# Kernel tuning notes

Measured on AMD Instinct MI355X. Metric: run time of the kernel, lower is better.

## Reference

```python
import jax, jax.numpy as jnp
import numpy as np

CODE_DIMS = [256, 512, 1024, 2048]
C = 256
BETA = 0.25
B = 64
N = 1024


def setup_inputs() -> dict:
    key = jax.random.key(0)
    ks = jax.random.split(key, 2 + len(CODE_DIMS))
    z_e = jax.random.normal(ks[0], (B, N, C), dtype=jnp.float32)
    expert_idx = jax.random.randint(ks[1], (B,), 0, len(CODE_DIMS))
    s = 1.0 / np.sqrt(C)  # torch uniform init bound
    inp = {"z_e": z_e, "expert_idx": expert_idx}
    for r, K in enumerate(CODE_DIMS):
        inp[f"cb{r}"] = jax.random.uniform(ks[2 + r], (K, C), minval=-s, maxval=s, dtype=jnp.float32)
    return inp


def _vq_expert(z_e, cb):
    # z_e: [B, N, C], cb: [K, C]
    Bz, Nz, Cz = z_e.shape
    zf = z_e.reshape(-1, Cz)                                  # [B*N, C]
    dists = ((zf ** 2).sum(axis=1, keepdims=True)
             + (cb ** 2).sum(axis=1)[None, :]
             - 2.0 * zf @ cb.T)                               # [B*N, K]
    idx = jnp.argmin(dists, axis=1)                           # [B*N]
    z_q = cb[idx].reshape(Bz, Nz, Cz)                         # [B, N, C]
    return z_q, idx.reshape(Bz, Nz)


def reference(z_e, expert_idx, cb0, cb1, cb2, cb3):
    cbs = [cb0, cb1, cb2, cb3]
    Bz, Nz, Cz = z_e.shape
    sg = jax.lax.stop_gradient
    z_q_out = jnp.zeros_like(z_e)
    indices = jnp.zeros((Bz, Nz), dtype=jnp.int32)
    vq_loss = jnp.asarray(0.0, dtype=z_e.dtype)
    for r, cb in enumerate(cbs):
        z_q, idx = _vq_expert(z_e, cb)
        mask = expert_idx == r                                # [B]
        mf = mask.astype(z_e.dtype)[:, None, None]            # [B,1,1]
        cnt = mask.sum().astype(z_e.dtype)
        denom = jnp.maximum(cnt * Nz * Cz, 1.0)               # mean over masked subset
        codebook_loss = jnp.sum(mf * (sg(z_q) - z_e) ** 2) / denom
        commit_loss = jnp.sum(mf * (z_q - sg(z_e)) ** 2) / denom
        loss_r = (codebook_loss + BETA * commit_loss) / Cz
        frac = cnt / Bz                                       # z_in.numel()/z_e.numel()
        vq_loss = vq_loss + frac * loss_r
        z_q_st = z_e + sg(z_q - z_e)                          # straight-through
        z_q_out = jnp.where(mf > 0, z_q_st, z_q_out)
        indices = jnp.where(mask[:, None], idx.astype(jnp.int32), indices)
    return z_q_out, indices, vq_loss
```

## Files before the change

### kernel.cpp

```cpp
#include <hip/hip_runtime.h>
#include <hip/hip_bf16.h>


#define EPS_GAP 2e-3f
#define NTOK 65536

typedef __attribute__((ext_vector_type(8))) short bf16x8;
typedef __attribute__((ext_vector_type(4))) float f32x4;

__device__ inline unsigned short f2bf(float f) {
  __hip_bfloat16 h = __float2bfloat16(f);
  unsigned short u;
  __builtin_memcpy(&u, &h, 2);
  return u;
}
__device__ inline float bf2f(unsigned short u) {
  return __uint_as_float(((unsigned)u) << 16);
}

__device__ inline void gll16(const unsigned short* g, unsigned short* l) {
  __builtin_amdgcn_global_load_lds(
      (const __attribute__((address_space(1))) unsigned int*)g,
      (__attribute__((address_space(3))) unsigned int*)l, 16, 0, 0);
}

__global__ __launch_bounds__(256) void csum_split_kernel(
    const float* __restrict__ cb0, const float* __restrict__ cb1,
    const float* __restrict__ cb2, const float* __restrict__ cb3,
    float* __restrict__ csums, double* __restrict__ csums64,
    unsigned short* __restrict__ cb_hi, unsigned short* __restrict__ cb_lo,
    int* __restrict__ wl_cnt) {
  if (blockIdx.x == 0 && threadIdx.x == 0) wl_cnt[0] = 0;
  int row = blockIdx.x * 4 + (threadIdx.x >> 6);
  int lane = threadIdx.x & 63;
  const float* src; int r;
  if (row < 256)       { src = cb0; r = row; }
  else if (row < 768)  { src = cb1; r = row - 256; }
  else if (row < 1792) { src = cb2; r = row - 768; }
  else                 { src = cb3; r = row - 1792; }
  float4 v = ((const float4*)(src + r * 256))[lane];
  unsigned short h0 = f2bf(v.x), h1 = f2bf(v.y), h2 = f2bf(v.z), h3 = f2bf(v.w);
  unsigned short l0 = f2bf(v.x - bf2f(h0)), l1 = f2bf(v.y - bf2f(h1));
  unsigned short l2 = f2bf(v.z - bf2f(h2)), l3 = f2bf(v.w - bf2f(h3));
  *(ushort4*)(cb_hi + (size_t)row * 256 + lane * 4) = make_ushort4(h0, h1, h2, h3);
  *(ushort4*)(cb_lo + (size_t)row * 256 + lane * 4) = make_ushort4(l0, l1, l2, l3);
  double s = (double)v.x*v.x + (double)v.y*v.y + (double)v.z*v.z + (double)v.w*v.w;
  #pragma unroll
  for (int off = 32; off >= 1; off >>= 1) s += __shfl_down(s, off, 64);
  if (lane == 0) { csums[row] = (float)s; csums64[row] = s; }
}

__global__ __launch_bounds__(256) void ze_split_kernel(
    const float* __restrict__ z, unsigned short* __restrict__ ze_hi,
    unsigned short* __restrict__ ze_lo, double* __restrict__ parts) {
  const float4* p = (const float4*)z;
  uint2* hi = (uint2*)ze_hi;
  uint2* lo = (uint2*)ze_lo;
  const int n4 = 4194304;
  double s = 0.0;
  for (int i = blockIdx.x * 256 + threadIdx.x; i < n4; i += 256 * 1024) {
    float4 v = p[i];
    unsigned hxy, hzw, lxy, lzw;
    asm("v_cvt_pk_bf16_f32 %0, %1, %2" : "=v"(hxy) : "v"(v.x), "v"(v.y));
    asm("v_cvt_pk_bf16_f32 %0, %1, %2" : "=v"(hzw) : "v"(v.z), "v"(v.w));
    float lx = v.x - __uint_as_float(hxy << 16);
    float ly = v.y - __uint_as_float(hxy & 0xffff0000u);
    float lz = v.z - __uint_as_float(hzw << 16);
    float lw = v.w - __uint_as_float(hzw & 0xffff0000u);
    asm("v_cvt_pk_bf16_f32 %0, %1, %2" : "=v"(lxy) : "v"(lx), "v"(ly));
    asm("v_cvt_pk_bf16_f32 %0, %1, %2" : "=v"(lzw) : "v"(lz), "v"(lw));
    hi[i] = make_uint2(hxy, hzw);
    lo[i] = make_uint2(lxy, lzw);
    s += (double)v.x*(double)v.x + (double)v.y*(double)v.y
       + (double)v.z*(double)v.z + (double)v.w*(double)v.w;
  }
  #pragma unroll
  for (int off = 32; off >= 1; off >>= 1) s += __shfl_down(s, off, 64);
  __shared__ double sh[4];
  if ((threadIdx.x & 63) == 0) sh[threadIdx.x >> 6] = s;
  __syncthreads();
  if (threadIdx.x == 0) parts[blockIdx.x] = sh[0] + sh[1] + sh[2] + sh[3];
}

__global__ __launch_bounds__(512, 4) void vq_mfma(
    const unsigned short* __restrict__ ze_hi, const unsigned short* __restrict__ ze_lo,
    const int* __restrict__ expert_idx,
    const unsigned short* __restrict__ cb_hi, const unsigned short* __restrict__ cb_lo,
    const float* __restrict__ csums,
    float* __restrict__ D1, int* __restrict__ K1, float* __restrict__ D2) {
  const int b  = blockIdx.y;
  const int e  = expert_idx[b];
  const int hc = blockIdx.z;
  if (hc >= (2 << e)) return;
  const int cs_off = (e == 0) ? 0 : (e == 1) ? 256 : (e == 2) ? 768 : 1792;
  const int krow0  = cs_off + hc * 128;
  const int t0     = b * 1024 + blockIdx.x * 128;

  __shared__ unsigned short smem[2 * 2 * 128 * 32];
  __shared__ float sh_cs[128];

  const int tid = threadIdx.x;
  if (tid < 128) sh_cs[tid] = csums[krow0 + tid];

  const int w = tid >> 6, l = tid & 63;
  const int h = w >> 1, q = w & 1;
  const int m16 = l & 15, g = l >> 4;

  const int srow   = w * 16 + (l >> 2);
  const int schunk = (l & 3) ^ ((srow >> 1) & 3);
  const size_t bsrc = (size_t)(krow0 + srow) * 256 + (size_t)schunk * 8;
  const int wslot = w * 512;

  const size_t a0 = (size_t)(t0 + h * 32 + m16) * 256 + (size_t)g * 8;
  const size_t a1 = a0 + 16 * 256;

  f32x4 acc[2][4];
  #pragma unroll
  for (int i = 0; i < 2; ++i)
    #pragma unroll
    for (int j = 0; j < 4; ++j) acc[i][j] = (f32x4){0.f, 0.f, 0.f, 0.f};

  bf16x8 pAh0, pAl0, pAh1, pAl1;
  bf16x8 qAh0, qAl0, qAh1, qAl1;

  pAh0 = *(const bf16x8*)(ze_hi + a0);
  pAl0 = *(const bf16x8*)(ze_lo + a0);
  pAh1 = *(const bf16x8*)(ze_hi + a1);
  pAl1 = *(const bf16x8*)(ze_lo + a1);
  gll16(cb_hi + bsrc, smem + wslot);
  gll16(cb_lo + bsrc, smem + 4096 + wslot);

#define VQ_STEP(KP, AH0, AL0, AH1, AL1, NH0, NL0, NH1, NL1)             \
  {                                                                     \
    unsigned short* buf_ = smem + ((KP) & 1) * 8192;                    \
    if ((KP) < 7) {                                                     \
      const int kcn_ = ((KP) + 1) * 32;                                 \
      unsigned short* nb_ = smem + (((KP) + 1) & 1) * 8192;             \
      gll16(cb_hi + bsrc + kcn_, nb_ + wslot);                          \
      gll16(cb_lo + bsrc + kcn_, nb_ + 4096 + wslot);                   \
      NH0 = *(const bf16x8*)(ze_hi + a0 + kcn_);                        \
      NL0 = *(const bf16x8*)(ze_lo + a0 + kcn_);                        \
      NH1 = *(const bf16x8*)(ze_hi + a1 + kcn_);                        \
      NL1 = *(const bf16x8*)(ze_lo + a1 + kcn_);                        \
      __builtin_amdgcn_sched_barrier(0);                                \
      asm volatile("s_waitcnt vmcnt(6)" ::: "memory");                  \
    } else {                                                            \
      asm volatile("s_waitcnt vmcnt(0)" ::: "memory");                  \
    }                                                                   \
    __builtin_amdgcn_s_barrier();                                       \
    _Pragma("unroll")                                                   \
    for (int j = 0; j < 4; ++j) {                                       \
      int row_ = q * 64 + j * 16 + m16;                                 \
      int n_ = row_ * 32 + ((g ^ ((row_ >> 1) & 3)) << 3);              \
      bf16x8 bh_ = *(bf16x8*)(buf_ + n_);                               \
      bf16x8 bl_ = *(bf16x8*)(buf_ + 4096 + n_);                        \
      acc[0][j] = __builtin_amdgcn_mfma_f32_16x16x32_bf16(bh_, AH0, acc[0][j], 0, 0, 0); \
      acc[0][j] = __builtin_amdgcn_mfma_f32_16x16x32_bf16(bl_, AH0, acc[0][j], 0, 0, 0); \
      acc[0][j] = __builtin_amdgcn_mfma_f32_16x16x32_bf16(bh_, AL0, acc[0][j], 0, 0, 0); \
      acc[1][j] = __builtin_amdgcn_mfma_f32_16x16x32_bf16(bh_, AH1, acc[1][j], 0, 0, 0); \
      acc[1][j] = __builtin_amdgcn_mfma_f32_16x16x32_bf16(bl_, AH1, acc[1][j], 0, 0, 0); \
      acc[1][j] = __builtin_amdgcn_mfma_f32_16x16x32_bf16(bh_, AL1, acc[1][j], 0, 0, 0); \
    }                                                                   \
    __builtin_amdgcn_sched_barrier(0);                                  \
    __builtin_amdgcn_s_barrier();                                       \
  }

  VQ_STEP(0, pAh0, pAl0, pAh1, pAl1, qAh0, qAl0, qAh1, qAl1)
  VQ_STEP(1, qAh0, qAl0, qAh1, qAl1, pAh0, pAl0, pAh1, pAl1)
  VQ_STEP(2, pAh0, pAl0, pAh1, pAl1, qAh0, qAl0, qAh1, qAl1)
  VQ_STEP(3, qAh0, qAl0, qAh1, qAl1, pAh0, pAl0, pAh1, pAl1)
  VQ_STEP(4, pAh0, pAl0, pAh1, pAl1, qAh0, qAl0, qAh1, qAl1)
  VQ_STEP(5, qAh0, qAl0, qAh1, qAl1, pAh0, pAl0, pAh1, pAl1)
  VQ_STEP(6, pAh0, pAl0, pAh1, pAl1, qAh0, qAl0, qAh1, qAl1)
  VQ_STEP(7, qAh0, qAl0, qAh1, qAl1, pAh0, pAl0, pAh1, pAl1)
#undef VQ_STEP

  __syncthreads();
  float* mD = (float*)smem;
  int*   mK = (int*)(smem + 512);
  float* mS = (float*)(smem + 1024);

  float cst[16];
  #pragma unroll
  for (int j = 0; j < 4; ++j)
    #pragma unroll
    for (int r = 0; r < 4; ++r)
      cst[j * 4 + r] = sh_cs[q * 64 + j * 16 + g * 4 + r];

  #pragma unroll
  for (int i = 0; i < 2; ++i) {
    float bv = 3.4e38f, sv = 3.4e38f; int bk = 0;
    #pragma unroll
    for (int j = 0; j < 4; ++j) {
      #pragma unroll
      for (int r = 0; r < 4; ++r) {
        float d = fmaf(-2.0f, acc[i][j][r], cst[j * 4 + r]);
        int   c = q * 64 + j * 16 + g * 4 + r;
        if (d < bv) { sv = bv; bv = d; bk = c; }
        else        { sv = fminf(sv, d); }
      }
    }
    #pragma unroll
    for (int off = 16; off <= 32; off <<= 1) {
      float ov = __shfl_xor(bv, off);
      int   ok = __shfl_xor(bk, off);
      float os = __shfl_xor(sv, off);
      float nb; int nk;
      if (ov < bv || (ov == bv && ok < bk)) { nb = ov; nk = ok; }
      else                                  { nb = bv; nk = bk; }
      sv = fminf(fmaxf(bv, ov), fminf(sv, os));
      bv = nb; bk = nk;
    }
    if (g == 0) {
      int tloc = h * 32 + i * 16 + m16;
      mD[tloc * 2 + q] = bv;
      mK[tloc * 2 + q] = bk;
      mS[tloc * 2 + q] = sv;
    }
  }
  __syncthreads();
  if (tid < 128) {
    float B = 3.4e38f, S = 3.4e38f; int Kb = 0;
    #pragma unroll
    for (int c = 0; c < 2; ++c) {
      float d1v = mD[tid * 2 + c];
      int   k1v = mK[tid * 2 + c];
      float d2v = mS[tid * 2 + c];
      S = fminf(fmaxf(B, d1v), fminf(S, d2v));
      if (d1v < B) { B = d1v; Kb = k1v; }
    }
    int tg = t0 + tid;
    D1[hc * NTOK + tg] = B;
    K1[hc * NTOK + tg] = hc * 128 + Kb;
    D2[hc * NTOK + tg] = S;
  }
}

__global__ __launch_bounds__(256) void combine_kernel(
    const int* __restrict__ expert_idx,
    const float* __restrict__ D1, const int* __restrict__ K1,
    const float* __restrict__ D2,
    const float* __restrict__ cb0, const float* __restrict__ cb1,
    const float* __restrict__ cb2, const float* __restrict__ cb3,
    float* __restrict__ idx_out,
    int* __restrict__ wl, int* __restrict__ wl_cnt,
    double* __restrict__ parts, float* __restrict__ zq_out) {
  __shared__ int sh_idx[256];
  __shared__ double shp[4];
  const int bid = blockIdx.x;
  const int t = bid * 256 + threadIdx.x;
  const int e = expert_idx[bid >> 2];
  const int nch = 2 << e;
  float B = 3.4e38f, S = 3.4e38f; int Kb = 0;
  for (int c = 0; c < nch; ++c) {
    float d1 = D1[c * NTOK + t];
    int   k1 = K1[c * NTOK + t];
    float d2 = D2[c * NTOK + t];
    S = fminf(fmaxf(B, d1), fminf(S, d2));
    if (d1 < B) { B = d1; Kb = k1; }
  }
  idx_out[t] = (float)Kb;
  sh_idx[threadIdx.x] = Kb;
  if (S - B < EPS_GAP) {
    int p = atomicAdd(wl_cnt, 1);
    wl[p] = t;
  }
  double s = (double)B;
  #pragma unroll
  for (int off = 32; off >= 1; off >>= 1) s += __shfl_down(s, off, 64);
  if ((threadIdx.x & 63) == 0) shp[threadIdx.x >> 6] = s;
  __syncthreads();
  if (threadIdx.x == 0) parts[bid] = shp[0] + shp[1] + shp[2] + shp[3];

  const float* cb = (e == 0) ? cb0 : (e == 1) ? cb1 : (e == 2) ? cb2 : cb3;
  const int wid = threadIdx.x >> 6, lane = threadIdx.x & 63;
  for (int it = 0; it < 64; ++it) {
    int tl = it * 4 + wid;
    int row = sh_idx[tl];
    ((float4*)(zq_out + (size_t)(bid * 256 + tl) * 256))[lane] =
        ((const float4*)(cb + (size_t)row * 256))[lane];
  }
}

__global__ __launch_bounds__(256) void rescue_kernel(
    const float* __restrict__ z_e, const int* __restrict__ expert_idx,
    const float* __restrict__ cb0, const float* __restrict__ cb1,
    const float* __restrict__ cb2, const float* __restrict__ cb3,
    const double* __restrict__ csums64,
    const int* __restrict__ wl, const int* __restrict__ wl_cnt,
    float* __restrict__ zq_out, float* __restrict__ idx_out) {
  __shared__ float  szrow[256];
  __shared__ double szs[4];
  __shared__ float  sdv[3][256];
  __shared__ int    skv[3][256];
  __shared__ int    s_kc;
  const int tid = threadIdx.x;
  const int wid = tid >> 6, lane = tid & 63;
  const int n = wl_cnt[0];
  for (int it = blockIdx.x; it < n; it += gridDim.x) {
    const int t = wl[it];
    const int b = t >> 10;
    const int e = expert_idx[b];
    const int K = 256 << e;
    const float* cb = (e == 0) ? cb0 : (e == 1) ? cb1 : (e == 2) ? cb2 : cb3;
    const int off = (e == 0) ? 0 : (e == 1) ? 256 : (e == 2) ? 768 : 1792;
    const double* cs64 = csums64 + off;

    __syncthreads();
    float zv = z_e[(size_t)t * 256 + tid];
    szrow[tid] = zv;
    double zsq = (double)zv * (double)zv;
    #pragma unroll
    for (int o = 32; o >= 1; o >>= 1) zsq += __shfl_down(zsq, o, 64);
    if (lane == 0) szs[wid] = zsq;
    __syncthreads();
    const float zs_mid = (float)(szs[0] + szs[1] + szs[2] + szs[3]);
    const unsigned zu = __float_as_uint(zs_mid);
    float zs[3] = {__uint_as_float(zu - 1), zs_mid, __uint_as_float(zu + 1)};

    float bd[3] = {3.4e38f, 3.4e38f, 3.4e38f};
    int   bk[3] = {1 << 30, 1 << 30, 1 << 30};
    const float4* z4 = (const float4*)szrow;
    for (int k = tid; k < K; k += 256) {
      const float4* c4 = (const float4*)(cb + (size_t)k * 256);
      double d0 = 0.0, d1v = 0.0, d2v = 0.0, d3 = 0.0;
      for (int qq = 0; qq < 64; qq += 4) {
        float4 a0 = z4[qq],     c0 = c4[qq];
        float4 a1 = z4[qq + 1], c1 = c4[qq + 1];
        float4 a2 = z4[qq + 2], c2 = c4[qq + 2];
        float4 a3 = z4[qq + 3], c3 = c4[qq + 3];
        d0 += (double)a0.x*c0.x + (double)a0.y*c0.y + (double)a0.z*c0.z + (double)a0.w*c0.w;
        d1v+= (double)a1.x*c1.x + (double)a1.y*c1.y + (double)a1.z*c1.z + (double)a1.w*c1.w;
        d2v+= (double)a2.x*c2.x + (double)a2.y*c2.y + (double)a2.z*c2.z + (double)a2.w*c2.w;
        d3 += (double)a3.x*c3.x + (double)a3.y*c3.y + (double)a3.z*c3.z + (double)a3.w*c3.w;
      }
      double dot = (d0 + d1v) + (d2v + d3);
      const float c32 = (float)cs64[k];
      const float m2d = (float)(2.0 * dot);
      #pragma unroll
      for (int v = 0; v < 3; ++v) {
        float T1  = zs[v] + c32;
        float d32 = T1 - m2d;
        if (d32 < bd[v]) { bd[v] = d32; bk[v] = k; }
      }
    }
    #pragma unroll
    for (int v = 0; v < 3; ++v) { sdv[v][tid] = bd[v]; skv[v][tid] = bk[v]; }
    __syncthreads();
    for (int s = 128; s >= 1; s >>= 1) {
      if (tid < s) {
        #pragma unroll
        for (int v = 0; v < 3; ++v) {
          float od = sdv[v][tid + s]; int ok = skv[v][tid + s];
          if (od < sdv[v][tid] || (od == sdv[v][tid] && ok < skv[v][tid])) {
            sdv[v][tid] = od; skv[v][tid] = ok;
          }
        }
      }
      __syncthreads();
    }
    if (tid == 0) {
      int k0 = skv[0][0], k1 = skv[1][0], k2 = skv[2][0];
      int kc = (k0 == k2) ? k0 : k1;
      s_kc = kc;
      idx_out[t] = (float)kc;
    }
    __syncthreads();
    const int kc = s_kc;
    if (tid < 64)
      ((float4*)(zq_out + (size_t)t * 256))[tid] =
          ((const float4*)(cb + (size_t)kc * 256))[tid];
  }
}

__global__ __launch_bounds__(256) void finalize_kernel(
    const double* __restrict__ parts_comb, const double* __restrict__ parts_zsq,
    float* __restrict__ loss_out) {
  const int tid = threadIdx.x;
  double s = parts_comb[tid] + parts_zsq[tid] + parts_zsq[tid + 256]
           + parts_zsq[tid + 512] + parts_zsq[tid + 768];
  #pragma unroll
  for (int off = 32; off >= 1; off >>= 1) s += __shfl_down(s, off, 64);
  __shared__ double sh[4];
  if ((tid & 63) == 0) sh[tid >> 6] = s;
  __syncthreads();
  if (tid == 0)
    loss_out[0] = (float)((sh[0] + sh[1] + sh[2] + sh[3]) * (1.25 / 4294967296.0));
}

extern "C" void kernel_launch(void* const* d_in, const int* in_sizes, int n_in,
                              void* d_out, int out_size, void* d_ws, size_t ws_size,
                              hipStream_t stream) {
  const float* z_e  = (const float*)d_in[0];
  const int*   eidx = (const int*)d_in[1];
  const float* cb0  = (const float*)d_in[2];
  const float* cb1  = (const float*)d_in[3];
  const float* cb2  = (const float*)d_in[4];
  const float* cb3  = (const float*)d_in[5];

  float* zq    = (float*)d_out;
  float* idxf  = (float*)d_out + 16777216;
  float* lossf = (float*)d_out + 16777216 + 65536;

  unsigned short* ze_hi = (unsigned short*)d_out;
  unsigned short* ze_lo = ze_hi + 16777216;

  char* wsp = (char*)d_ws;
  double*         parts_comb = (double*)wsp;           wsp += 256 * 8;
  double*         parts_zsq  = (double*)wsp;           wsp += 1024 * 8;
  double*         csums64    = (double*)wsp;           wsp += 3840 * 8;
  float*          csums      = (float*)wsp;            wsp += 3840 * 4;
  int*            wl_cnt     = (int*)wsp;              wsp += 16;
  int*            wl         = (int*)wsp;              wsp += NTOK * 4;
  unsigned short* cb_hi      = (unsigned short*)wsp;   wsp += 3840 * 256 * 2;
  unsigned short* cb_lo      = (unsigned short*)wsp;   wsp += 3840 * 256 * 2;
  float*          D1         = (float*)wsp;            wsp += 16 * NTOK * 4;
  int*            K1         = (int*)wsp;              wsp += 16 * NTOK * 4;
  float*          D2         = (float*)wsp;            wsp += 16 * NTOK * 4;

  csum_split_kernel<<<960, 256, 0, stream>>>(cb0, cb1, cb2, cb3,
                                             csums, csums64, cb_hi, cb_lo, wl_cnt);
  ze_split_kernel<<<1024, 256, 0, stream>>>(z_e, ze_hi, ze_lo, parts_zsq);
  dim3 grid(8, 64, 16);
  vq_mfma<<<grid, 512, 0, stream>>>(ze_hi, ze_lo, eidx, cb_hi, cb_lo, csums, D1, K1, D2);
  combine_kernel<<<256, 256, 0, stream>>>(eidx, D1, K1, D2, cb0, cb1, cb2, cb3,
                                          idxf, wl, wl_cnt, parts_comb, zq);
  rescue_kernel<<<2048, 256, 0, stream>>>(z_e, eidx, cb0, cb1, cb2, cb3,
                                          csums64, wl, wl_cnt, zq, idxf);
  finalize_kernel<<<1, 256, 0, stream>>>(parts_comb, parts_zsq, lossf);
}
```

Before: 403.1 us.

## Bucket rescue worklist per expert and batch eight tokens per block

The near-tie worklist is now split into per-expert buckets, so the rescue kernel handles eight tokens that share a codebook in each block. Every codebook row it loads from global memory is reused across those eight tokens instead of being fetched once per token. In exchange it adds a serial per-block z-squared sum, eight sequential block reductions per batch, and larger register arrays that may lower occupancy. The grid is also halved.

```diff
diff --git a/kernel.cpp b/kernel.cpp
--- a/kernel.cpp
+++ b/kernel.cpp
@@ -30,7 +30,7 @@
     float* __restrict__ csums, double* __restrict__ csums64,
     unsigned short* __restrict__ cb_hi, unsigned short* __restrict__ cb_lo,
     int* __restrict__ wl_cnt) {
-  if (blockIdx.x == 0 && threadIdx.x == 0) wl_cnt[0] = 0;
+  if (blockIdx.x == 0 && threadIdx.x < 4) wl_cnt[threadIdx.x] = 0;
   int row = blockIdx.x * 4 + (threadIdx.x >> 6);
   int lane = threadIdx.x & 63;
   const float* src; int r;
@@ -262,8 +262,8 @@
   idx_out[t] = (float)Kb;
   sh_idx[threadIdx.x] = Kb;
   if (S - B < EPS_GAP) {
-    int p = atomicAdd(wl_cnt, 1);
-    wl[p] = t;
+    int p = atomicAdd(wl_cnt + e, 1);
+    wl[e * NTOK + p] = t;
   }
   double s = (double)B;
   #pragma unroll
@@ -283,93 +283,120 @@
 }
 
 __global__ __launch_bounds__(256) void rescue_kernel(
-    const float* __restrict__ z_e, const int* __restrict__ expert_idx,
+    const float* __restrict__ z_e,
     const float* __restrict__ cb0, const float* __restrict__ cb1,
     const float* __restrict__ cb2, const float* __restrict__ cb3,
     const double* __restrict__ csums64,
     const int* __restrict__ wl, const int* __restrict__ wl_cnt,
     float* __restrict__ zq_out, float* __restrict__ idx_out) {
-  __shared__ float  szrow[256];
-  __shared__ double szs[4];
+  __shared__ float  szrow[8 * 256];
+  __shared__ double szs[8];
+  __shared__ int    stok[8];
   __shared__ float  sdv[3][256];
   __shared__ int    skv[3][256];
   __shared__ int    s_kc;
   const int tid = threadIdx.x;
-  const int wid = tid >> 6, lane = tid & 63;
-  const int n = wl_cnt[0];
-  for (int it = blockIdx.x; it < n; it += gridDim.x) {
-    const int t = wl[it];
-    const int b = t >> 10;
-    const int e = expert_idx[b];
+
+  for (int e = 0; e < 4; ++e) {
+    const int n_e = wl_cnt[e];
+    if (n_e == 0) continue;
     const int K = 256 << e;
     const float* cb = (e == 0) ? cb0 : (e == 1) ? cb1 : (e == 2) ? cb2 : cb3;
     const int off = (e == 0) ? 0 : (e == 1) ? 256 : (e == 2) ? 768 : 1792;
     const double* cs64 = csums64 + off;
-
-    __syncthreads();
-    float zv = z_e[(size_t)t * 256 + tid];
-    szrow[tid] = zv;
-    double zsq = (double)zv * (double)zv;
-    #pragma unroll
-    for (int o = 32; o >= 1; o >>= 1) zsq += __shfl_down(zsq, o, 64);
-    if (lane == 0) szs[wid] = zsq;
-    __syncthreads();
-    const float zs_mid = (float)(szs[0] + szs[1] + szs[2] + szs[3]);
-    const unsigned zu = __float_as_uint(zs_mid);
-    float zs[3] = {__uint_as_float(zu - 1), zs_mid, __uint_as_float(zu + 1)};
-
-    float bd[3] = {3.4e38f, 3.4e38f, 3.4e38f};
-    int   bk[3] = {1 << 30, 1 << 30, 1 << 30};
-    const float4* z4 = (const float4*)szrow;
-    for (int k = tid; k < K; k += 256) {
-      const float4* c4 = (const float4*)(cb + (size_t)k * 256);
-      double d0 = 0.0, d1v = 0.0, d2v = 0.0, d3 = 0.0;
-      for (int qq = 0; qq < 64; qq += 4) {
-        float4 a0 = z4[qq],     c0 = c4[qq];
-        float4 a1 = z4[qq + 1], c1 = c4[qq + 1];
-        float4 a2 = z4[qq + 2], c2 = c4[qq + 2];
-        float4 a3 = z4[qq + 3], c3 = c4[qq + 3];
-        d0 += (double)a0.x*c0.x + (double)a0.y*c0.y + (double)a0.z*c0.z + (double)a0.w*c0.w;
-        d1v+= (double)a1.x*c1.x + (double)a1.y*c1.y + (double)a1.z*c1.z + (double)a1.w*c1.w;
-        d2v+= (double)a2.x*c2.x + (double)a2.y*c2.y + (double)a2.z*c2.z + (double)a2.w*c2.w;
-        d3 += (double)a3.x*c3.x + (double)a3.y*c3.y + (double)a3.z*c3.z + (double)a3.w*c3.w;
+    const int nb = (n_e + 7) >> 3;
+
+    for (int bi = blockIdx.x; bi < nb; bi += gridDim.x) {
+      const int m = min(8, n_e - bi * 8);
+      __syncthreads();
+      if (tid < 8) stok[tid] = (tid < m) ? wl[e * NTOK + bi * 8 + tid] : wl[e * NTOK + bi * 8];
+      __syncthreads();
+      #pragma unroll
+      for (int r = 0; r < 8; ++r)
+        szrow[r * 256 + tid] = z_e[(size_t)stok[r] * 256 + tid];
+      __syncthreads();
+      if (tid < 8) {
+        double s = 0.0;
+        for (int i = 0; i < 256; ++i) {
+          double v = (double)szrow[tid * 256 + i];
+          s += v * v;
+        }
+        szs[tid] = s;
       }
-      double dot = (d0 + d1v) + (d2v + d3);
-      const float c32 = (float)cs64[k];
-      const float m2d = (float)(2.0 * dot);
+      __syncthreads();
+      unsigned zu[8];
       #pragma unroll
-      for (int v = 0; v < 3; ++v) {
-        float T1  = zs[v] + c32;
-        float d32 = T1 - m2d;
-        if (d32 < bd[v]) { bd[v] = d32; bk[v] = k; }
-      }
-    }
-    #pragma unroll
-    for (int v = 0; v < 3; ++v) { sdv[v][tid] = bd[v]; skv[v][tid] = bk[v]; }
-    __syncthreads();
-    for (int s = 128; s >= 1; s >>= 1) {
-      if (tid < s) {
+      for (int r = 0; r < 8; ++r) zu[r] = __float_as_uint((float)szs[r]);
+
+      float bd[3][8]; int bk[3][8];
+      #pragma unroll
+      for (int v = 0; v < 3; ++v)
         #pragma unroll
-        for (int v = 0; v < 3; ++v) {
-          float od = sdv[v][tid + s]; int ok = skv[v][tid + s];
-          if (od < sdv[v][tid] || (od == sdv[v][tid] && ok < skv[v][tid])) {
-            sdv[v][tid] = od; skv[v][tid] = ok;
+        for (int r = 0; r < 8; ++r) { bd[v][r] = 3.4e38f; bk[v][r] = 1 << 30; }
+
+      const float4* z4 = (const float4*)szrow;
+      for (int k = tid; k < K; k += 256) {
+        const float4* c4 = (const float4*)(cb + (size_t)k * 256);
+        double acc[8];
+        #pragma unroll
+        for (int r = 0; r < 8; ++r) acc[r] = 0.0;
+        for (int qq = 0; qq < 64; qq += 2) {
+          float4 cv0 = c4[qq], cv1 = c4[qq + 1];
+          #pragma unroll
+          for (int r = 0; r < 8; ++r) {
+            float4 zv0 = z4[r * 64 + qq];
+            float4 zv1 = z4[r * 64 + qq + 1];
+            acc[r] += (double)zv0.x*cv0.x + (double)zv0.y*cv0.y
+                    + (double)zv0.z*cv0.z + (double)zv0.w*cv0.w
+                    + (double)zv1.x*cv1.x + (double)zv1.y*cv1.y
+                    + (double)zv1.z*cv1.z + (double)zv1.w*cv1.w;
+          }
+        }
+        const float c32 = (float)cs64[k];
+        #pragma unroll
+        for (int r = 0; r < 8; ++r) {
+          const float m2d = (float)(2.0 * acc[r]);
+          #pragma unroll
+          for (int v = 0; v < 3; ++v) {
+            float zsv = __uint_as_float(zu[r] + (unsigned)(v - 1));
+            float T1  = zsv + c32;
+            float d32 = T1 - m2d;
+            if (d32 < bd[v][r]) { bd[v][r] = d32; bk[v][r] = k; }
           }
         }
       }
-      __syncthreads();
+
+      for (int r = 0; r < m; ++r) {
+        #pragma unroll
+        for (int v = 0; v < 3; ++v) { sdv[v][tid] = bd[v][r]; skv[v][tid] = bk[v][r]; }
+        __syncthreads();
+        for (int s = 128; s >= 1; s >>= 1) {
+          if (tid < s) {
+            #pragma unroll
+            for (int v = 0; v < 3; ++v) {
+              float od = sdv[v][tid + s]; int ok = skv[v][tid + s];
+              if (od < sdv[v][tid] || (od == sdv[v][tid] && ok < skv[v][tid])) {
+                sdv[v][tid] = od; skv[v][tid] = ok;
+              }
+            }
+          }
+          __syncthreads();
+        }
+        const int t = stok[r];
+        if (tid == 0) {
+          int k0 = skv[0][0], k1 = skv[1][0], k2 = skv[2][0];
+          int kc = (k0 == k2) ? k0 : k1;
+          s_kc = kc;
+          idx_out[t] = (float)kc;
+        }
+        __syncthreads();
+        const int kc = s_kc;
+        if (tid < 64)
+          ((float4*)(zq_out + (size_t)t * 256))[tid] =
+              ((const float4*)(cb + (size_t)kc * 256))[tid];
+        __syncthreads();
+      }
     }
-    if (tid == 0) {
-      int k0 = skv[0][0], k1 = skv[1][0], k2 = skv[2][0];
-      int kc = (k0 == k2) ? k0 : k1;
-      s_kc = kc;
-      idx_out[t] = (float)kc;
-    }
-    __syncthreads();
-    const int kc = s_kc;
-    if (tid < 64)
-      ((float4*)(zq_out + (size_t)t * 256))[tid] =
-          ((const float4*)(cb + (size_t)kc * 256))[tid];
   }
 }
 
@@ -411,7 +438,7 @@
   double*         csums64    = (double*)wsp;           wsp += 3840 * 8;
   float*          csums      = (float*)wsp;            wsp += 3840 * 4;
   int*            wl_cnt     = (int*)wsp;              wsp += 16;
-  int*            wl         = (int*)wsp;              wsp += NTOK * 4;
+  int*            wl         = (int*)wsp;              wsp += NTOK * 16;
   unsigned short* cb_hi      = (unsigned short*)wsp;   wsp += 3840 * 256 * 2;
   unsigned short* cb_lo      = (unsigned short*)wsp;   wsp += 3840 * 256 * 2;
   float*          D1         = (float*)wsp;            wsp += 16 * NTOK * 4;
@@ -425,7 +452,7 @@
   vq_mfma<<<grid, 512, 0, stream>>>(ze_hi, ze_lo, eidx, cb_hi, cb_lo, csums, D1, K1, D2);
   combine_kernel<<<256, 256, 0, stream>>>(eidx, D1, K1, D2, cb0, cb1, cb2, cb3,
                                           idxf, wl, wl_cnt, parts_comb, zq);
-  rescue_kernel<<<2048, 256, 0, stream>>>(z_e, eidx, cb0, cb1, cb2, cb3,
+  rescue_kernel<<<1024, 256, 0, stream>>>(z_e, cb0, cb1, cb2, cb3,
                                           csums64, wl, wl_cnt, zq, idxf);
   finalize_kernel<<<1, 256, 0, stream>>>(parts_comb, parts_zsq, lossf);
 }
```

Measured after the change: 747.2 us. +85.4%, slower.
